# Kernel tuning notes

Hardware: AMD Instinct MI355X
Metric: run time of the kernel (lower is better)

## Reference

```python
import jax, jax.numpy as jnp
import numpy as np

N0, N1, N2, K, D, H = 131072, 16384, 4096, 8, 256, 256
LN_EPS = 1e-5
BN_EPS = 1e-5


def _lstm_last(x, W_ih, W_hh, b_ih, b_hh):
    # x: [N, K, Din]; returns final hidden state [N, Hh] (DGL lstm aggregator)
    N = x.shape[0]
    Hh = W_hh.shape[1]

    def step(carry, xt):
        h, c = carry
        z = xt @ W_ih.T + b_ih + h @ W_hh.T + b_hh  # [N, 4*Hh]
        i, f, g, o = jnp.split(z, 4, axis=-1)
        c = jax.nn.sigmoid(f) * c + jax.nn.sigmoid(i) * jnp.tanh(g)
        h = jax.nn.sigmoid(o) * jnp.tanh(c)
        return (h, c), None

    init = (jnp.zeros((N, Hh), x.dtype), jnp.zeros((N, Hh), x.dtype))
    (h, _), _ = jax.lax.scan(step, init, jnp.swapaxes(x, 0, 1))
    return h


def _sage_lstm(h_src, idx, W_ih, W_hh, b_ih, b_hh, W_self, W_neigh, b_neigh):
    # DGL SAGEConv(aggregator='lstm'), eval mode (feat_drop = identity).
    n_dst = idx.shape[0]
    h_self = h_src[:n_dst]                  # DGL block: dst nodes are first rows of src
    nbrs = jnp.take(h_src, idx, axis=0)     # [n_dst, K, Din] neighbor gather
    h_n = _lstm_last(nbrs, W_ih, W_hh, b_ih, b_hh)
    # fc_self has no bias, fc_neigh has bias (DGL); activation = exact GELU
    return jax.nn.gelu(h_self @ W_self.T + h_n @ W_neigh.T + b_neigh, approximate=False)


def _layernorm(x, g, b):
    mu = jnp.mean(x, -1, keepdims=True)
    var = jnp.mean((x - mu) ** 2, -1, keepdims=True)
    return (x - mu) * jax.lax.rsqrt(var + LN_EPS) * g + b


def _forward(h0, idx0, idx1,
             W_ih1, W_hh1, b_ih1, b_hh1, W_self1, W_neigh1, b_neigh1,
             W_ih2, W_hh2, b_ih2, b_hh2, W_self2, W_neigh2, b_neigh2,
             ln_g, ln_b, bn_g, bn_b, bn_mean, bn_var, W1, b1, W2, b2):
    h = _sage_lstm(h0, idx0, W_ih1, W_hh1, b_ih1, b_hh1, W_self1, W_neigh1, b_neigh1)
    h = _layernorm(h, ln_g, ln_b)           # shared self.norm
    h = _sage_lstm(h, idx1, W_ih2, W_hh2, b_ih2, b_hh2, W_self2, W_neigh2, b_neigh2)
    h = _layernorm(h, ln_g, ln_b)
    # classifier head, eval mode: Dropout = identity, BatchNorm1d uses running stats
    h = (h - bn_mean) * jax.lax.rsqrt(bn_var + BN_EPS) * bn_g + bn_b
    h = jax.nn.gelu(h @ W1.T + b1, approximate=False)
    return h @ W2.T + b2                    # [N2, 1] logits


def setup_inputs() -> dict:
    key = jax.random.key(0)
    ks = jax.random.split(key, 24)

    def p(i, shape, scale=0.05):
        return jax.random.normal(ks[i], shape, jnp.float32) * scale

    return {
        "h0": jax.random.normal(ks[0], (N0, D), jnp.float32),
        "idx0": jax.random.randint(ks[1], (N1, K), 0, N0),
        "idx1": jax.random.randint(ks[2], (N2, K), 0, N1),
        "W_ih1": p(3, (4 * H, D)), "W_hh1": p(4, (4 * H, H)),
        "b_ih1": p(5, (4 * H,)), "b_hh1": p(6, (4 * H,)),
        "W_self1": p(7, (H, D)), "W_neigh1": p(8, (H, H)), "b_neigh1": p(9, (H,)),
        "W_ih2": p(10, (4 * H, H)), "W_hh2": p(11, (4 * H, H)),
        "b_ih2": p(12, (4 * H,)), "b_hh2": p(13, (4 * H,)),
        "W_self2": p(14, (H, H)), "W_neigh2": p(15, (H, H)), "b_neigh2": p(16, (H,)),
        "ln_g": jnp.ones((H,), jnp.float32), "ln_b": jnp.zeros((H,), jnp.float32),
        "bn_g": jnp.ones((H,), jnp.float32), "bn_b": jnp.zeros((H,), jnp.float32),
        "bn_mean": p(17, (H,)), "bn_var": jnp.ones((H,), jnp.float32),
        "W1": p(18, (H, H)), "b1": p(19, (H,)),
        "W2": p(20, (1, H)), "b2": p(21, (1,)),
    }


def reference(h0, idx0, idx1,
              W_ih1, W_hh1, b_ih1, b_hh1, W_self1, W_neigh1, b_neigh1,
              W_ih2, W_hh2, b_ih2, b_hh2, W_self2, W_neigh2, b_neigh2,
              ln_g, ln_b, bn_g, bn_b, bn_mean, bn_var, W1, b1, W2, b2):
    return _forward(h0, idx0, idx1,
                    W_ih1, W_hh1, b_ih1, b_hh1, W_self1, W_neigh1, b_neigh1,
                    W_ih2, W_hh2, b_ih2, b_hh2, W_self2, W_neigh2, b_neigh2,
                    ln_g, ln_b, bn_g, bn_b, bn_mean, bn_var, W1, b1, W2, b2)
```

## Files before the change

kernel.cpp:

```cpp
#include <hip/hip_runtime.h>
#include <hip/hip_bf16.h>
#include <math.h>

#define PN0 131072
#define PN1 16384
#define PN2 4096
#define PK  8

typedef __attribute__((ext_vector_type(8))) short short8;
typedef __attribute__((ext_vector_type(4))) float f32x4;

__device__ __forceinline__ unsigned pkbf2(float a, float b) {
  unsigned ua = __float_as_uint(a); ua = (ua + 0x7FFFu + ((ua >> 16) & 1u)) >> 16;
  unsigned ub = __float_as_uint(b); ub = (ub + 0x7FFFu + ((ub >> 16) & 1u)) >> 16;
  return ua | (ub << 16);
}
__device__ __forceinline__ unsigned short bf16r(float a) {
  unsigned ua = __float_as_uint(a);
  return (unsigned short)((ua + 0x7FFFu + ((ua >> 16) & 1u)) >> 16);
}
__device__ __forceinline__ float sigf(float x) { return 1.f / (1.f + __expf(-x)); }
__device__ __forceinline__ float tanh_fast(float x) { return 1.f - 2.f / (__expf(2.f * x) + 1.f); }

__device__ __forceinline__ void gload16(const void* g, void* l) {
  __builtin_amdgcn_global_load_lds(
      (const __attribute__((address_space(1))) void*)g,
      (__attribute__((address_space(3))) void*)l, 16, 0, 0);
}

__device__ __forceinline__ void dev_cvt_perm(int t, unsigned short* dst,
                                             const float* src) {
  int row = t >> 3, c0 = (t & 7) * 32;
  const float* s = src + (size_t)row * 256 + c0;
  unsigned short* d = dst + (size_t)row * 256 + c0;
  float f[32];
#pragma unroll
  for (int i = 0; i < 8; ++i) *(float4*)&f[i * 4] = *(const float4*)(s + i * 4);
#pragma unroll
  for (int q = 0; q < 4; ++q) {
    uint4 u;
    u.x = pkbf2(f[4 * q + 0], f[4 * q + 1]);
    u.y = pkbf2(f[4 * q + 2], f[4 * q + 3]);
    u.z = pkbf2(f[16 + 4 * q + 0], f[16 + 4 * q + 1]);
    u.w = pkbf2(f[16 + 4 * q + 2], f[16 + 4 * q + 3]);
    *(uint4*)(d + q * 8) = u;
  }
}

__device__ __forceinline__ void dev_pack_w(int t, unsigned short* dst,
                                           const float* Wih, const float* Whh) {
  int e = t & 7, slot = (t >> 3) & 3, row = (t >> 5) & 127;
  int kc = (t >> 12) & 15, tn = t >> 16;
  int q = slot ^ ((row >> 1) & 3);
  int k = kc * 32 + 16 * (e >> 2) + 4 * q + (e & 3);
  int hc = tn * 32 + ((row >> 6) << 4) + (row & 15);
  int g = (row >> 4) & 3;
  int n = g * 256 + hc;
  float v = (k < 256) ? Wih[(size_t)n * 256 + k] : Whh[(size_t)n * 256 + (k - 256)];
  dst[t] = bf16r(v);
}

__device__ __forceinline__ void dev_pack_plain(int t, unsigned short* dst,
                                               const float* A, const float* B, int nkc) {
  int e = t & 7, slot = (t >> 3) & 3, row = (t >> 5) & 127;
  int rest = t >> 12;
  int kc = rest % nkc, tn = rest / nkc;
  int q = slot ^ ((row >> 1) & 3);
  int k = kc * 32 + 16 * (e >> 2) + 4 * q + (e & 3);
  int n = tn * 128 + row;
  float v = (k < 256) ? A[(size_t)n * 256 + k] : B[(size_t)n * 256 + (k - 256)];
  dst[t] = bf16r(v);
}

__global__ __launch_bounds__(256) void prep_kernel(
    unsigned short* __restrict__ h0b, const float* __restrict__ h0,
    unsigned short* __restrict__ pB1, const float* __restrict__ Wih1, const float* __restrict__ Whh1,
    unsigned short* __restrict__ pB2, const float* __restrict__ Wih2, const float* __restrict__ Whh2,
    unsigned short* __restrict__ pC1, const float* __restrict__ Ws1, const float* __restrict__ Wn1,
    unsigned short* __restrict__ pC2, const float* __restrict__ Ws2, const float* __restrict__ Wn2,
    unsigned short* __restrict__ pM, const float* __restrict__ W1,
    float* __restrict__ bcat1, const float* __restrict__ bih1, const float* __restrict__ bhh1,
    float* __restrict__ bcat2, const float* __restrict__ bih2, const float* __restrict__ bhh2)
{
  const int b = blockIdx.x;
  const int tid = threadIdx.x;
  if (b < 4096) {
    dev_cvt_perm(b * 256 + tid, h0b, h0);
  } else if (b < 6144) {
    dev_pack_w((b - 4096) * 256 + tid, pB1, Wih1, Whh1);
  } else if (b < 8192) {
    dev_pack_w((b - 6144) * 256 + tid, pB2, Wih2, Whh2);
  } else if (b < 8704) {
    dev_pack_plain((b - 8192) * 256 + tid, pC1, Ws1, Wn1, 16);
  } else if (b < 9216) {
    dev_pack_plain((b - 8704) * 256 + tid, pC2, Ws2, Wn2, 16);
  } else if (b < 9472) {
    dev_pack_plain((b - 9216) * 256 + tid, pM, W1, W1, 8);
  } else {
    int i = (b - 9472) * 256 + tid;
    if (i < 1024) bcat1[i] = bih1[i] + bhh1[i];
    else          bcat2[i - 1024] = bih2[i - 1024] + bhh2[i - 1024];
  }
}

template<int MI>
__global__ __launch_bounds__(256) void lstm_step_t(
    const unsigned short* __restrict__ xb,
    const int* __restrict__ idx, int t,
    const unsigned short* __restrict__ hb_in,
    const unsigned short* __restrict__ packW,
    const float* __restrict__ bcat,
    float* __restrict__ cbuf,
    unsigned short* __restrict__ hb_out,
    int first)
{
  __shared__ short As[2][MI * 1024];
  __shared__ short Bs[2][4096];

  const int tid = threadIdx.x;
  const int l = tid & 63;
  const int w = tid >> 6;
  const int m0 = blockIdx.x * (MI * 32);
  const int tn = blockIdx.y;
  const int wm = w >> 1, wn = w & 1;

  const int q = (l & 3) ^ ((l >> 3) & 3);
  const int r0 = w * (MI * 8) + (l >> 2);
  const int m_a = m0 + r0;
  const unsigned short* xp0 = xb + (size_t)idx[(size_t)m_a * PK + t] * 256 + 8 * q;
  const unsigned short* hp0 = hb_in + (size_t)m_a * 256 + 8 * q;
  const unsigned short* xp1 = nullptr;
  const unsigned short* hp1 = nullptr;
  if constexpr (MI == 4) {
    const int m_b = m_a + 16;
    xp1 = xb + (size_t)idx[(size_t)m_b * PK + t] * 256 + 8 * q;
    hp1 = hb_in + (size_t)m_b * 256 + 8 * q;
  }
  const unsigned short* bp = packW + (size_t)tn * 65536 + (size_t)w * 1024 + (size_t)l * 8;

  f32x4 acc[MI][4];
#pragma unroll
  for (int mi = 0; mi < MI; ++mi)
#pragma unroll
    for (int ni = 0; ni < 4; ++ni) acc[mi][ni] = (f32x4)(0.f);

  auto STAGE = [&](int buf, int kc) {
    short* Ad = &As[buf][0];
    short* Bd = &Bs[buf][0];
    gload16(bp + (size_t)kc * 4096, Bd + w * 1024);
    gload16(bp + (size_t)kc * 4096 + 512, Bd + w * 1024 + 512);
    const unsigned short* s0 = (kc < 8) ? xp0 + kc * 32 : hp0 + (kc - 8) * 32;
    gload16(s0, Ad + w * (MI * 256));
    if constexpr (MI == 4) {
      const unsigned short* s1 = (kc < 8) ? xp1 + kc * 32 : hp1 + (kc - 8) * 32;
      gload16(s1, Ad + w * 1024 + 512);
    }
  };

  const int lr = l & 15;
  const int lq = l >> 4;
  const int slot_r = (lq ^ ((l >> 1) & 3)) * 8;

  auto COMPUTE = [&](int buf) {
    short8 af[MI], bf[4];
#pragma unroll
    for (int mi = 0; mi < MI; ++mi)
      af[mi] = *(const short8*)&As[buf][(wm * (MI * 16) + mi * 16 + lr) * 32 + slot_r];
#pragma unroll
    for (int ni = 0; ni < 4; ++ni)
      bf[ni] = *(const short8*)&Bs[buf][(wn * 64 + ni * 16 + lr) * 32 + slot_r];
#pragma unroll
    for (int mi = 0; mi < MI; ++mi)
#pragma unroll
      for (int ni = 0; ni < 4; ++ni)
        acc[mi][ni] = __builtin_amdgcn_mfma_f32_16x16x32_bf16(af[mi], bf[ni], acc[mi][ni], 0, 0, 0);
  };

  const int NK = first ? 8 : 16;
  STAGE(0, 0);
  __syncthreads();
  for (int kc = 0; kc < NK; ++kc) {
    const int cur = kc & 1;
    if (kc + 1 < NK) STAGE(cur ^ 1, kc + 1);
    COMPUTE(cur);
    __syncthreads();
  }

  const int hc = tn * 32 + wn * 16 + lr;
  const float bi = bcat[hc], bff = bcat[256 + hc], bg = bcat[512 + hc], bo = bcat[768 + hc];
  const int kl = hc & 31;
  const int hpos = (hc & ~31) + ((kl >> 2) & 3) * 8 + ((kl >> 4) & 1) * 4 + (kl & 3);
#pragma unroll
  for (int mi = 0; mi < MI; ++mi) {
#pragma unroll
    for (int r = 0; r < 4; ++r) {
      const int m = m0 + wm * (MI * 16) + mi * 16 + lq * 4 + r;
      const size_t off = (size_t)m * 256;
      const float zi = acc[mi][0][r] + bi;
      const float zf = acc[mi][1][r] + bff;
      const float zg = acc[mi][2][r] + bg;
      const float zo = acc[mi][3][r] + bo;
      const float cp = first ? 0.f : cbuf[off + hc];
      const float cn = sigf(zf) * cp + sigf(zi) * tanh_fast(zg);
      const float hn = sigf(zo) * tanh_fast(cn);
      cbuf[off + hc] = cn;
      hb_out[off + hpos] = bf16r(hn);
    }
  }
}

__global__ __launch_bounds__(256) void gemm_bf16_kernel(
    const unsigned short* __restrict__ selfb,
    const unsigned short* __restrict__ neighb,
    const unsigned short* __restrict__ packW,
    const float* __restrict__ bias,
    float* __restrict__ out, int NK, int do_gelu)
{
  __shared__ short As[2][2048];
  __shared__ short Bs[2][4096];

  const int tid = threadIdx.x;
  const int l = tid & 63;
  const int w = tid >> 6;
  const int m0 = blockIdx.x * 64;
  const int tn = blockIdx.y;
  const int wm = w >> 1, wn = w & 1;

  const int q = (l & 3) ^ ((l >> 3) & 3);
  const int r0 = w * 16 + (l >> 2);
  const int m_a = m0 + r0;
  const unsigned short* sp0 = selfb + (size_t)m_a * 256 + 8 * q;
  const unsigned short* np0 = neighb ? neighb + (size_t)m_a * 256 + 8 * q : sp0;
  const unsigned short* bp = packW + (size_t)tn * 4096 * NK + (size_t)w * 1024 + (size_t)l * 8;

  f32x4 acc[2][4];
#pragma unroll
  for (int mi = 0; mi < 2; ++mi)
#pragma unroll
    for (int ni = 0; ni < 4; ++ni) acc[mi][ni] = (f32x4)(0.f);

  auto STAGE = [&](int buf, int kc) {
    short* Ad = &As[buf][0];
    short* Bd = &Bs[buf][0];
    gload16(bp + (size_t)kc * 4096, Bd + w * 1024);
    gload16(bp + (size_t)kc * 4096 + 512, Bd + w * 1024 + 512);
    const unsigned short* s0 = (kc < 8) ? sp0 + kc * 32 : np0 + (kc - 8) * 32;
    gload16(s0, Ad + w * 512);
  };

  const int lr = l & 15;
  const int lq = l >> 4;
  const int slot_r = (lq ^ ((l >> 1) & 3)) * 8;

  auto COMPUTE = [&](int buf) {
    short8 af[2], bf[4];
#pragma unroll
    for (int mi = 0; mi < 2; ++mi)
      af[mi] = *(const short8*)&As[buf][(wm * 32 + mi * 16 + lr) * 32 + slot_r];
#pragma unroll
    for (int ni = 0; ni < 4; ++ni)
      bf[ni] = *(const short8*)&Bs[buf][(wn * 64 + ni * 16 + lr) * 32 + slot_r];
#pragma unroll
    for (int mi = 0; mi < 2; ++mi)
#pragma unroll
      for (int ni = 0; ni < 4; ++ni)
        acc[mi][ni] = __builtin_amdgcn_mfma_f32_16x16x32_bf16(af[mi], bf[ni], acc[mi][ni], 0, 0, 0);
  };

  STAGE(0, 0);
  __syncthreads();
  for (int kc = 0; kc < NK; ++kc) {
    const int cur = kc & 1;
    if (kc + 1 < NK) STAGE(cur ^ 1, kc + 1);
    COMPUTE(cur);
    __syncthreads();
  }

#pragma unroll
  for (int mi = 0; mi < 2; ++mi) {
#pragma unroll
    for (int ni = 0; ni < 4; ++ni) {
      const int n = tn * 128 + wn * 64 + ni * 16 + lr;
      const float bb = bias[n];
#pragma unroll
      for (int r = 0; r < 4; ++r) {
        const int m = m0 + wm * 32 + mi * 16 + lq * 4 + r;
        float v = acc[mi][ni][r] + bb;
        if (do_gelu) v = 0.5f * v * (1.f + erff(v * 0.70710678118654752f));
        out[(size_t)m * 256 + n] = v;
      }
    }
  }
}

__global__ __launch_bounds__(256) void ln_bn_kernel(
    const float* __restrict__ in, unsigned short* __restrict__ outb,
    const float* __restrict__ g, const float* __restrict__ b,
    const float* bnm, const float* bnv, const float* bng, const float* bnb,
    int do_bn)
{
  const int row = blockIdx.x * 4 + (threadIdx.x >> 6);
  const int lane = threadIdx.x & 63;
  const int c = lane * 4;
  float4 v = *(const float4*)(in + (size_t)row * 256 + c);
  float s = v.x + v.y + v.z + v.w;
  float qq = v.x * v.x + v.y * v.y + v.z * v.z + v.w * v.w;
#pragma unroll
  for (int o = 32; o > 0; o >>= 1) { s += __shfl_xor(s, o); qq += __shfl_xor(qq, o); }
  const float mu = s * (1.f / 256.f);
  const float var = qq * (1.f / 256.f) - mu * mu;
  const float rs = rsqrtf(var + 1e-5f);
  float vv[4] = { v.x, v.y, v.z, v.w };
  float y[4];
#pragma unroll
  for (int j = 0; j < 4; ++j) {
    float t = (vv[j] - mu) * rs * g[c + j] + b[c + j];
    if (do_bn) t = (t - bnm[c + j]) * rsqrtf(bnv[c + j] + 1e-5f) * bng[c + j] + bnb[c + j];
    y[j] = t;
  }
  const int base = (c & ~31) + (((c >> 2) & 3) * 8) + (((c >> 4) & 1) * 4);
  uint2 u = make_uint2(pkbf2(y[0], y[1]), pkbf2(y[2], y[3]));
  *(uint2*)(outb + (size_t)row * 256 + base) = u;
}

__global__ __launch_bounds__(256) void head_kernel(
    const float* __restrict__ h4, const float* __restrict__ W2,
    const float* __restrict__ b2, float* __restrict__ out)
{
  const int row = blockIdx.x * 4 + (threadIdx.x >> 6);
  const int lane = threadIdx.x & 63;
  float4 a = *(const float4*)(h4 + (size_t)row * 256 + lane * 4);
  float4 w = *(const float4*)(W2 + lane * 4);
  float s = a.x * w.x + a.y * w.y + a.z * w.z + a.w * w.w;
#pragma unroll
  for (int o = 32; o > 0; o >>= 1) s += __shfl_xor(s, o);
  if (lane == 0) out[row] = s + b2[0];
}

extern "C" void kernel_launch(void* const* d_in, const int* in_sizes, int n_in,
                              void* d_out, int out_size, void* d_ws, size_t ws_size,
                              hipStream_t stream) {
  const float* h0       = (const float*)d_in[0];
  const int*   idx0     = (const int*)  d_in[1];
  const int*   idx1     = (const int*)  d_in[2];
  const float* W_ih1    = (const float*)d_in[3];
  const float* W_hh1    = (const float*)d_in[4];
  const float* b_ih1    = (const float*)d_in[5];
  const float* b_hh1    = (const float*)d_in[6];
  const float* W_self1  = (const float*)d_in[7];
  const float* W_neigh1 = (const float*)d_in[8];
  const float* b_neigh1 = (const float*)d_in[9];
  const float* W_ih2    = (const float*)d_in[10];
  const float* W_hh2    = (const float*)d_in[11];
  const float* b_ih2    = (const float*)d_in[12];
  const float* b_hh2    = (const float*)d_in[13];
  const float* W_self2  = (const float*)d_in[14];
  const float* W_neigh2 = (const float*)d_in[15];
  const float* b_neigh2 = (const float*)d_in[16];
  const float* ln_g     = (const float*)d_in[17];
  const float* ln_b     = (const float*)d_in[18];
  const float* bn_g     = (const float*)d_in[19];
  const float* bn_b     = (const float*)d_in[20];
  const float* bn_mean  = (const float*)d_in[21];
  const float* bn_var   = (const float*)d_in[22];
  const float* W1       = (const float*)d_in[23];
  const float* b1       = (const float*)d_in[24];
  const float* W2       = (const float*)d_in[25];
  const float* b2       = (const float*)d_in[26];
  float* out = (float*)d_out;

  float* ws = (float*)d_ws;
  unsigned short* packB1 = (unsigned short*)ws;
  unsigned short* packB2 = (unsigned short*)(ws + 262144);
  unsigned short* packC1 = (unsigned short*)(ws + 524288);
  unsigned short* packC2 = (unsigned short*)(ws + 589824);
  unsigned short* packM  = (unsigned short*)(ws + 655360);
  float* bcat1 = ws + 688128;
  float* bcat2 = bcat1 + 1024;
  unsigned short* h0b = (unsigned short*)(bcat2 + 1024);
  float* afterh0 = (float*)h0b + 16777216;
  unsigned short* hbA = (unsigned short*)afterh0;
  unsigned short* hbB = (unsigned short*)(afterh0 + 2097152);
  float* cbuf = afterh0 + 4194304;
  float* sbuf = cbuf + 4194304;
  unsigned short* h1b = (unsigned short*)(sbuf + 4194304);
  unsigned short* h3b = (unsigned short*)(sbuf + 4194304 + 2097152);
  float* h4 = sbuf + 4194304 + 2097152 + 524288;

  prep_kernel<<<9480, 256, 0, stream>>>(
      h0b, h0,
      packB1, W_ih1, W_hh1,
      packB2, W_ih2, W_hh2,
      packC1, W_self1, W_neigh1,
      packC2, W_self2, W_neigh2,
      packM, W1,
      bcat1, b_ih1, b_hh1,
      bcat2, b_ih2, b_hh2);

  for (int t = 0; t < PK; ++t) {
    unsigned short* hin  = (t & 1) ? hbA : hbB;
    unsigned short* hout = (t & 1) ? hbB : hbA;
    lstm_step_t<4><<<dim3(PN1 / 128, 8), 256, 0, stream>>>(
        h0b, idx0, t, hin, packB1, bcat1, cbuf, hout, t == 0);
  }
  gemm_bf16_kernel<<<dim3(PN1 / 64, 2), 256, 0, stream>>>(h0b, hbB, packC1, b_neigh1,
                                                          sbuf, 16, 1);
  ln_bn_kernel<<<PN1 / 4, 256, 0, stream>>>(sbuf, h1b, ln_g, ln_b,
                                            nullptr, nullptr, nullptr, nullptr, 0);

  for (int t = 0; t < PK; ++t) {
    unsigned short* hin  = (t & 1) ? hbA : hbB;
    unsigned short* hout = (t & 1) ? hbB : hbA;
    lstm_step_t<2><<<dim3(PN2 / 64, 8), 256, 0, stream>>>(
        h1b, idx1, t, hin, packB2, bcat2, cbuf, hout, t == 0);
  }
  gemm_bf16_kernel<<<dim3(PN2 / 64, 2), 256, 0, stream>>>(h1b, hbB, packC2, b_neigh2,
                                                          sbuf, 16, 1);
  ln_bn_kernel<<<PN2 / 4, 256, 0, stream>>>(sbuf, h3b, ln_g, ln_b,
                                            bn_mean, bn_var, bn_g, bn_b, 1);
  gemm_bf16_kernel<<<dim3(PN2 / 64, 2), 256, 0, stream>>>(h3b, nullptr, packM, b1,
                                                          h4, 8, 1);
  head_kernel<<<PN2 / 4, 256, 0, stream>>>(h4, W2, b2, out);
}
```

Baseline: 476.7 us.

## Fuse combine GEMM with LayerNorm and MLP with head; triple-buffer LSTM steps

Replaces the separate combine GEMM plus LayerNorm/BatchNorm kernels with one kernel. Each block computes all 256 output columns for 32 rows, so it can reduce row statistics in-register and through LDS, and the fp32 intermediate buffer is no longer written to or read from memory. The classifier GEMM and the dot-product head are fused in the same way. Separately, the LSTM step kernel moves to a three-stage LDS pipeline with explicit vmcnt waits and raw barriers, so loads are issued two chunks ahead. The tradeoff is more LDS per block and hand-counted wait values that must match the number of loads issued per stage.

Result: no change. 475.2 us (-0.3%).

```diff
diff --git a/kernel.cpp b/kernel.cpp
--- a/kernel.cpp
+++ b/kernel.cpp
@@ -21,6 +21,12 @@
 }
 __device__ __forceinline__ float sigf(float x) { return 1.f / (1.f + __expf(-x)); }
 __device__ __forceinline__ float tanh_fast(float x) { return 1.f - 2.f / (__expf(2.f * x) + 1.f); }
+__device__ __forceinline__ float gelu_f(float v) {
+  return 0.5f * v * (1.f + erff(v * 0.70710678118654752f));
+}
+__device__ __forceinline__ int permc(int n) {
+  return (n & ~31) + (((n >> 2) & 3) * 8) + (((n >> 4) & 1) * 4) + (n & 3);
+}
 
 __device__ __forceinline__ void gload16(const void* g, void* l) {
   __builtin_amdgcn_global_load_lds(
@@ -114,8 +120,8 @@
     unsigned short* __restrict__ hb_out,
     int first)
 {
-  __shared__ short As[2][MI * 1024];
-  __shared__ short Bs[2][4096];
+  __shared__ short As[3][MI * 1024];
+  __shared__ short Bs[3][4096];
 
   const int tid = threadIdx.x;
   const int l = tid & 63;
@@ -178,18 +184,29 @@
 
   const int NK = first ? 8 : 16;
   STAGE(0, 0);
-  __syncthreads();
+  STAGE(1, 1);
   for (int kc = 0; kc < NK; ++kc) {
-    const int cur = kc & 1;
-    if (kc + 1 < NK) STAGE(cur ^ 1, kc + 1);
-    COMPUTE(cur);
-    __syncthreads();
+    const int b0 = kc % 3;
+    if (kc + 2 < NK) {
+      STAGE((kc + 2) % 3, kc + 2);
+      if constexpr (MI == 4) asm volatile("s_waitcnt vmcnt(8)" ::: "memory");
+      else                   asm volatile("s_waitcnt vmcnt(6)" ::: "memory");
+    } else if (kc + 1 < NK) {
+      if constexpr (MI == 4) asm volatile("s_waitcnt vmcnt(4)" ::: "memory");
+      else                   asm volatile("s_waitcnt vmcnt(3)" ::: "memory");
+    } else {
+      asm volatile("s_waitcnt vmcnt(0)" ::: "memory");
+    }
+    __builtin_amdgcn_s_barrier();
+    asm volatile("" ::: "memory");
+    COMPUTE(b0);
+    asm volatile("" ::: "memory");
+    if (kc + 1 < NK) __builtin_amdgcn_s_barrier();
   }
 
   const int hc = tn * 32 + wn * 16 + lr;
   const float bi = bcat[hc], bff = bcat[256 + hc], bg = bcat[512 + hc], bo = bcat[768 + hc];
-  const int kl = hc & 31;
-  const int hpos = (hc & ~31) + ((kl >> 2) & 3) * 8 + ((kl >> 4) & 1) * 4 + (kl & 3);
+  const int hpos = permc(hc);
 #pragma unroll
   for (int mi = 0; mi < MI; ++mi) {
 #pragma unroll
@@ -209,132 +226,213 @@
   }
 }
 
-__global__ __launch_bounds__(256) void gemm_bf16_kernel(
+__global__ __launch_bounds__(256) void combine_ln_kernel(
     const unsigned short* __restrict__ selfb,
     const unsigned short* __restrict__ neighb,
     const unsigned short* __restrict__ packW,
     const float* __restrict__ bias,
-    float* __restrict__ out, int NK, int do_gelu)
-{
-  __shared__ short As[2][2048];
-  __shared__ short Bs[2][4096];
-
-  const int tid = threadIdx.x;
-  const int l = tid & 63;
-  const int w = tid >> 6;
-  const int m0 = blockIdx.x * 64;
-  const int tn = blockIdx.y;
-  const int wm = w >> 1, wn = w & 1;
-
-  const int q = (l & 3) ^ ((l >> 3) & 3);
-  const int r0 = w * 16 + (l >> 2);
-  const int m_a = m0 + r0;
-  const unsigned short* sp0 = selfb + (size_t)m_a * 256 + 8 * q;
-  const unsigned short* np0 = neighb ? neighb + (size_t)m_a * 256 + 8 * q : sp0;
-  const unsigned short* bp = packW + (size_t)tn * 4096 * NK + (size_t)w * 1024 + (size_t)l * 8;
-
-  f32x4 acc[2][4];
-#pragma unroll
-  for (int mi = 0; mi < 2; ++mi)
-#pragma unroll
-    for (int ni = 0; ni < 4; ++ni) acc[mi][ni] = (f32x4)(0.f);
-
-  auto STAGE = [&](int buf, int kc) {
-    short* Ad = &As[buf][0];
-    short* Bd = &Bs[buf][0];
-    gload16(bp + (size_t)kc * 4096, Bd + w * 1024);
-    gload16(bp + (size_t)kc * 4096 + 512, Bd + w * 1024 + 512);
-    const unsigned short* s0 = (kc < 8) ? sp0 + kc * 32 : np0 + (kc - 8) * 32;
-    gload16(s0, Ad + w * 512);
-  };
-
-  const int lr = l & 15;
-  const int lq = l >> 4;
-  const int slot_r = (lq ^ ((l >> 1) & 3)) * 8;
-
-  auto COMPUTE = [&](int buf) {
-    short8 af[2], bf[4];
-#pragma unroll
-    for (int mi = 0; mi < 2; ++mi)
-      af[mi] = *(const short8*)&As[buf][(wm * 32 + mi * 16 + lr) * 32 + slot_r];
-#pragma unroll
-    for (int ni = 0; ni < 4; ++ni)
-      bf[ni] = *(const short8*)&Bs[buf][(wn * 64 + ni * 16 + lr) * 32 + slot_r];
-#pragma unroll
-    for (int mi = 0; mi < 2; ++mi)
-#pragma unroll
-      for (int ni = 0; ni < 4; ++ni)
-        acc[mi][ni] = __builtin_amdgcn_mfma_f32_16x16x32_bf16(af[mi], bf[ni], acc[mi][ni], 0, 0, 0);
-  };
-
-  STAGE(0, 0);
-  __syncthreads();
-  for (int kc = 0; kc < NK; ++kc) {
-    const int cur = kc & 1;
-    if (kc + 1 < NK) STAGE(cur ^ 1, kc + 1);
-    COMPUTE(cur);
-    __syncthreads();
-  }
-
-#pragma unroll
-  for (int mi = 0; mi < 2; ++mi) {
-#pragma unroll
-    for (int ni = 0; ni < 4; ++ni) {
-      const int n = tn * 128 + wn * 64 + ni * 16 + lr;
-      const float bb = bias[n];
-#pragma unroll
-      for (int r = 0; r < 4; ++r) {
-        const int m = m0 + wm * 32 + mi * 16 + lq * 4 + r;
-        float v = acc[mi][ni][r] + bb;
-        if (do_gelu) v = 0.5f * v * (1.f + erff(v * 0.70710678118654752f));
-        out[(size_t)m * 256 + n] = v;
-      }
-    }
-  }
-}
-
-__global__ __launch_bounds__(256) void ln_bn_kernel(
-    const float* __restrict__ in, unsigned short* __restrict__ outb,
+    unsigned short* __restrict__ outb,
     const float* __restrict__ g, const float* __restrict__ b,
     const float* bnm, const float* bnv, const float* bng, const float* bnb,
     int do_bn)
 {
-  const int row = blockIdx.x * 4 + (threadIdx.x >> 6);
-  const int lane = threadIdx.x & 63;
-  const int c = lane * 4;
-  float4 v = *(const float4*)(in + (size_t)row * 256 + c);
-  float s = v.x + v.y + v.z + v.w;
-  float qq = v.x * v.x + v.y * v.y + v.z * v.z + v.w * v.w;
-#pragma unroll
-  for (int o = 32; o > 0; o >>= 1) { s += __shfl_xor(s, o); qq += __shfl_xor(qq, o); }
-  const float mu = s * (1.f / 256.f);
-  const float var = qq * (1.f / 256.f) - mu * mu;
-  const float rs = rsqrtf(var + 1e-5f);
-  float vv[4] = { v.x, v.y, v.z, v.w };
-  float y[4];
-#pragma unroll
-  for (int j = 0; j < 4; ++j) {
-    float t = (vv[j] - mu) * rs * g[c + j] + b[c + j];
-    if (do_bn) t = (t - bnm[c + j]) * rsqrtf(bnv[c + j] + 1e-5f) * bng[c + j] + bnb[c + j];
-    y[j] = t;
-  }
-  const int base = (c & ~31) + (((c >> 2) & 3) * 8) + (((c >> 4) & 1) * 4);
-  uint2 u = make_uint2(pkbf2(y[0], y[1]), pkbf2(y[2], y[3]));
-  *(uint2*)(outb + (size_t)row * 256 + base) = u;
-}
-
-__global__ __launch_bounds__(256) void head_kernel(
-    const float* __restrict__ h4, const float* __restrict__ W2,
-    const float* __restrict__ b2, float* __restrict__ out)
+  __shared__ short As[2][1024];
+  __shared__ short Bs[2][8192];
+
+  const int tid = threadIdx.x;
+  const int l = tid & 63;
+  const int w = tid >> 6;
+  const int m0 = blockIdx.x * 32;
+  const int wm = w >> 1, wn = w & 1;
+
+  const int q = (l & 3) ^ ((l >> 3) & 3);
+  const int arow = (w & 1) * 16 + (l >> 2);
+  const unsigned short* sp = selfb + (size_t)(m0 + arow) * 256 + 8 * q;
+  const unsigned short* np = neighb + (size_t)(m0 + arow) * 256 + 8 * q;
+
+  f32x4 acc[8];
+#pragma unroll
+  for (int ni = 0; ni < 8; ++ni) acc[ni] = (f32x4)(0.f);
+
+  auto STAGE = [&](int buf, int kc) {
+    short* Ad = &As[buf][0];
+    short* Bd = &Bs[buf][0];
+#pragma unroll
+    for (int u = 0; u < 4; ++u) {
+      const int base = w * 64 + u * 16;
+      const int tile = base >> 7, r128b = base & 127;
+      gload16(packW + (size_t)tile * 65536 + (size_t)kc * 4096 + (size_t)r128b * 32 + (size_t)l * 8,
+              Bd + w * 2048 + u * 512);
+    }
+    if (w < 2) {
+      const unsigned short* s0 = (kc < 8) ? sp + kc * 32 : np + (kc - 8) * 32;
+      gload16(s0, Ad + w * 512);
+    }
+  };
+
+  const int lr = l & 15;
+  const int lq = l >> 4;
+  const int slot_r = (lq ^ ((l >> 1) & 3)) * 8;
+
+  auto COMPUTE = [&](int buf) {
+    short8 af = *(const short8*)&As[buf][(wm * 16 + lr) * 32 + slot_r];
+#pragma unroll
+    for (int ni = 0; ni < 8; ++ni) {
+      short8 bf = *(const short8*)&Bs[buf][(wn * 128 + ni * 16 + lr) * 32 + slot_r];
+      acc[ni] = __builtin_amdgcn_mfma_f32_16x16x32_bf16(af, bf, acc[ni], 0, 0, 0);
+    }
+  };
+
+  STAGE(0, 0);
+  __syncthreads();
+  for (int kc = 0; kc < 16; ++kc) {
+    const int cur = kc & 1;
+    if (kc + 1 < 16) STAGE(cur ^ 1, kc + 1);
+    COMPUTE(cur);
+    __syncthreads();
+  }
+
+  float val[8][4];
+  float s[4] = {0.f, 0.f, 0.f, 0.f}, qq[4] = {0.f, 0.f, 0.f, 0.f};
+#pragma unroll
+  for (int ni = 0; ni < 8; ++ni) {
+    const int n = wn * 128 + ni * 16 + lr;
+    const float bb = bias[n];
+#pragma unroll
+    for (int r = 0; r < 4; ++r) {
+      float v = gelu_f(acc[ni][r] + bb);
+      val[ni][r] = v;
+      s[r] += v;
+      qq[r] += v * v;
+    }
+  }
+#pragma unroll
+  for (int off = 1; off < 16; off <<= 1) {
+#pragma unroll
+    for (int r = 0; r < 4; ++r) {
+      s[r] += __shfl_xor(s[r], off);
+      qq[r] += __shfl_xor(qq[r], off);
+    }
+  }
+  float* sred = (float*)&As[0][0];
+  __syncthreads();
+  if (lr == 0) {
+#pragma unroll
+    for (int r = 0; r < 4; ++r) {
+      const int row = wm * 16 + lq * 4 + r;
+      sred[wn * 64 + row] = s[r];
+      sred[wn * 64 + 32 + row] = qq[r];
+    }
+  }
+  __syncthreads();
+#pragma unroll
+  for (int r = 0; r < 4; ++r) {
+    const int row = wm * 16 + lq * 4 + r;
+    const float S = sred[row] + sred[64 + row];
+    const float Q = sred[32 + row] + sred[96 + row];
+    const float mu = S * (1.f / 256.f);
+    const float var = Q * (1.f / 256.f) - mu * mu;
+    const float rs = rsqrtf(var + 1e-5f);
+    const int m = m0 + row;
+#pragma unroll
+    for (int ni = 0; ni < 8; ++ni) {
+      const int n = wn * 128 + ni * 16 + lr;
+      float y = (val[ni][r] - mu) * rs * g[n] + b[n];
+      if (do_bn) y = (y - bnm[n]) * rsqrtf(bnv[n] + 1e-5f) * bng[n] + bnb[n];
+      outb[(size_t)m * 256 + permc(n)] = bf16r(y);
+    }
+  }
+}
+
+__global__ __launch_bounds__(256) void mlp_head_kernel(
+    const unsigned short* __restrict__ h3b,
+    const unsigned short* __restrict__ packM,
+    const float* __restrict__ b1,
+    const float* __restrict__ W2, const float* __restrict__ b2,
+    float* __restrict__ out)
 {
-  const int row = blockIdx.x * 4 + (threadIdx.x >> 6);
-  const int lane = threadIdx.x & 63;
-  float4 a = *(const float4*)(h4 + (size_t)row * 256 + lane * 4);
-  float4 w = *(const float4*)(W2 + lane * 4);
-  float s = a.x * w.x + a.y * w.y + a.z * w.z + a.w * w.w;
-#pragma unroll
-  for (int o = 32; o > 0; o >>= 1) s += __shfl_xor(s, o);
-  if (lane == 0) out[row] = s + b2[0];
+  __shared__ short As[2][1024];
+  __shared__ short Bs[2][8192];
+
+  const int tid = threadIdx.x;
+  const int l = tid & 63;
+  const int w = tid >> 6;
+  const int m0 = blockIdx.x * 32;
+  const int wm = w >> 1, wn = w & 1;
+
+  const int q = (l & 3) ^ ((l >> 3) & 3);
+  const int arow = (w & 1) * 16 + (l >> 2);
+  const unsigned short* sp = h3b + (size_t)(m0 + arow) * 256 + 8 * q;
+
+  f32x4 acc[8];
+#pragma unroll
+  for (int ni = 0; ni < 8; ++ni) acc[ni] = (f32x4)(0.f);
+
+  auto STAGE = [&](int buf, int kc) {
+    short* Ad = &As[buf][0];
+    short* Bd = &Bs[buf][0];
+#pragma unroll
+    for (int u = 0; u < 4; ++u) {
+      const int base = w * 64 + u * 16;
+      const int tile = base >> 7, r128b = base & 127;
+      gload16(packM + (size_t)tile * 32768 + (size_t)kc * 4096 + (size_t)r128b * 32 + (size_t)l * 8,
+              Bd + w * 2048 + u * 512);
+    }
+    if (w < 2) gload16(sp + kc * 32, Ad + w * 512);
+  };
+
+  const int lr = l & 15;
+  const int lq = l >> 4;
+  const int slot_r = (lq ^ ((l >> 1) & 3)) * 8;
+
+  auto COMPUTE = [&](int buf) {
+    short8 af = *(const short8*)&As[buf][(wm * 16 + lr) * 32 + slot_r];
+#pragma unroll
+    for (int ni = 0; ni < 8; ++ni) {
+      short8 bf = *(const short8*)&Bs[buf][(wn * 128 + ni * 16 + lr) * 32 + slot_r];
+      acc[ni] = __builtin_amdgcn_mfma_f32_16x16x32_bf16(af, bf, acc[ni], 0, 0, 0);
+    }
+  };
+
+  STAGE(0, 0);
+  __syncthreads();
+  for (int kc = 0; kc < 8; ++kc) {
+    const int cur = kc & 1;
+    if (kc + 1 < 8) STAGE(cur ^ 1, kc + 1);
+    COMPUTE(cur);
+    __syncthreads();
+  }
+
+  float s[4] = {0.f, 0.f, 0.f, 0.f};
+#pragma unroll
+  for (int ni = 0; ni < 8; ++ni) {
+    const int n = wn * 128 + ni * 16 + lr;
+    const float bb = b1[n];
+    const float w2 = W2[n];
+#pragma unroll
+    for (int r = 0; r < 4; ++r) {
+      s[r] += gelu_f(acc[ni][r] + bb) * w2;
+    }
+  }
+#pragma unroll
+  for (int off = 1; off < 16; off <<= 1)
+#pragma unroll
+    for (int r = 0; r < 4; ++r) s[r] += __shfl_xor(s[r], off);
+
+  float* sred = (float*)&As[0][0];
+  __syncthreads();
+  if (lr == 0) {
+#pragma unroll
+    for (int r = 0; r < 4; ++r) sred[wn * 32 + wm * 16 + lq * 4 + r] = s[r];
+  }
+  __syncthreads();
+  if (wn == 0 && lr == 0) {
+#pragma unroll
+    for (int r = 0; r < 4; ++r) {
+      const int row = wm * 16 + lq * 4 + r;
+      out[m0 + row] = sred[row] + sred[32 + row] + b2[0];
+    }
+  }
 }
 
 extern "C" void kernel_launch(void* const* d_in, const int* in_sizes, int n_in,
@@ -382,10 +480,8 @@
   unsigned short* hbA = (unsigned short*)afterh0;
   unsigned short* hbB = (unsigned short*)(afterh0 + 2097152);
   float* cbuf = afterh0 + 4194304;
-  float* sbuf = cbuf + 4194304;
-  unsigned short* h1b = (unsigned short*)(sbuf + 4194304);
-  unsigned short* h3b = (unsigned short*)(sbuf + 4194304 + 2097152);
-  float* h4 = sbuf + 4194304 + 2097152 + 524288;
+  unsigned short* h1b = (unsigned short*)(cbuf + 4194304);
+  unsigned short* h3b = (unsigned short*)(cbuf + 4194304 + 2097152);
 
   prep_kernel<<<9480, 256, 0, stream>>>(
       h0b, h0,
@@ -403,10 +499,9 @@
     lstm_step_t<4><<<dim3(PN1 / 128, 8), 256, 0, stream>>>(
         h0b, idx0, t, hin, packB1, bcat1, cbuf, hout, t == 0);
   }
-  gemm_bf16_kernel<<<dim3(PN1 / 64, 2), 256, 0, stream>>>(h0b, hbB, packC1, b_neigh1,
-                                                          sbuf, 16, 1);
-  ln_bn_kernel<<<PN1 / 4, 256, 0, stream>>>(sbuf, h1b, ln_g, ln_b,
-                                            nullptr, nullptr, nullptr, nullptr, 0);
+  combine_ln_kernel<<<PN1 / 32, 256, 0, stream>>>(
+      h0b, hbB, packC1, b_neigh1, h1b, ln_g, ln_b,
+      nullptr, nullptr, nullptr, nullptr, 0);
 
   for (int t = 0; t < PK; ++t) {
     unsigned short* hin  = (t & 1) ? hbA : hbB;
@@ -414,11 +509,8 @@
     lstm_step_t<2><<<dim3(PN2 / 64, 8), 256, 0, stream>>>(
         h1b, idx1, t, hin, packB2, bcat2, cbuf, hout, t == 0);
   }
-  gemm_bf16_kernel<<<dim3(PN2 / 64, 2), 256, 0, stream>>>(h1b, hbB, packC2, b_neigh2,
-                                                          sbuf, 16, 1);
-  ln_bn_kernel<<<PN2 / 4, 256, 0, stream>>>(sbuf, h3b, ln_g, ln_b,
-                                            bn_mean, bn_var, bn_g, bn_b, 1);
-  gemm_bf16_kernel<<<dim3(PN2 / 64, 2), 256, 0, stream>>>(h3b, nullptr, packM, b1,
-                                                          h4, 8, 1);
-  head_kernel<<<PN2 / 4, 256, 0, stream>>>(h4, W2, b2, out);
-}
+  combine_ln_kernel<<<PN2 / 32, 256, 0, stream>>>(
+      h1b, hbB, packC2, b_neigh2, h3b, ln_g, ln_b,
+      bn_mean, bn_var, bn_g, bn_b, 1);
+  mlp_head_kernel<<<PN2 / 32, 256, 0, stream>>>(h3b, packM, b1, W2, b2, out);
+}
```
